# Kernel tuning notes

Measured on AMD Instinct MI355X. Metric: run time of the kernel, lower is better.

## Reference

```python
import jax, jax.numpy as jnp
import numpy as np

K, N = 4096, 4096
GROUP_SIZE = 64
N_GROUPS = N // GROUP_SIZE
B, S = 4, 2048
NBITS = 4


def setup_inputs() -> dict:
    key = jax.random.key(0)
    ks = jax.random.split(key, 7)
    x = jax.random.normal(ks[0], (B, S, N), dtype=jnp.float32)
    # per-group scales/zeros broadcast over the group_size axis
    scales = jax.random.uniform(ks[1], (K, N_GROUPS, 1), dtype=jnp.float32, minval=0.001, maxval=0.05)
    zeros = jax.random.uniform(ks[2], (K, N_GROUPS, 1), dtype=jnp.float32, minval=0.0, maxval=2.0 ** NBITS - 1)
    mu1 = jax.random.uniform(ks[3], (N,), dtype=jnp.float32, minval=0.5, maxval=1.5)
    mu2 = jax.random.uniform(ks[4], (K,), dtype=jnp.float32, minval=0.5, maxval=1.5)
    bias = jax.random.normal(ks[5], (K,), dtype=jnp.float32)
    W_q = jax.random.randint(ks[6], (K, N), 0, 2 ** NBITS, dtype=jnp.int32)
    return {"x": x, "scales": scales, "zeros": zeros, "mu1": mu1, "mu2": mu2, "bias": bias, "W_q": W_q}


def reference(x, scales, zeros, mu1, mu2, bias, W_q):
    # dequantize: per-group (Q - zero) * scale, then Sinkhorn rescale mu2 (rows) * mu1 (cols)
    k, n = W_q.shape
    n_groups = scales.shape[1]
    Qg = W_q.astype(jnp.float32).reshape(k, n_groups, -1)  # [K, G, gs]
    W_deq = ((Qg - zeros) * scales).reshape(k, n) * mu2[:, None] * mu1[None, :]
    W_deq = W_deq.astype(x.dtype)
    # nn.functional.linear: x @ W^T + b
    return jnp.einsum('bsn,kn->bsk', x, W_deq) + bias
```

## Files before the change

kernel.cpp:

```cpp
#include <hip/hip_runtime.h>
#include <hip/hip_bf16.h>
#include <stdint.h>
#include <type_traits>

typedef unsigned short u16;
typedef __bf16 bf16x8 __attribute__((ext_vector_type(8)));
typedef float f32x4 __attribute__((ext_vector_type(4)));

#define M_TOT 8192
#define N_TOT 4096
#define K_TOT 4096
#define BM 256
#define BN 256
#define BK 64
#define NT 64

#define HALF_EL 8192
#define B_OFF   16384
#define SLOT_EL 32768

template <int V> using ic = std::integral_constant<int, V>;
template <bool V> using bc = std::integral_constant<bool, V>;

__device__ __forceinline__ u16 f2bf(float f) {
    union { float f; uint32_t u; } v; v.f = f;
    uint32_t u = v.u;
    return (u16)((u + 0x7fffu + ((u >> 16) & 1u)) >> 16);
}

__global__ __launch_bounds__(256) void cvt_x_kernel(const float* __restrict__ x,
                                                    u16* __restrict__ xb) {
    const int i = blockIdx.x * blockDim.x + threadIdx.x;
    const float4* p = (const float4*)x + (size_t)i * 2;
    float4 v0 = p[0], v1 = p[1];
    uint4 o;
    o.x = (uint32_t)f2bf(v0.x) | ((uint32_t)f2bf(v0.y) << 16);
    o.y = (uint32_t)f2bf(v0.z) | ((uint32_t)f2bf(v0.w) << 16);
    o.z = (uint32_t)f2bf(v1.x) | ((uint32_t)f2bf(v1.y) << 16);
    o.w = (uint32_t)f2bf(v1.z) | ((uint32_t)f2bf(v1.w) << 16);
    *((uint4*)(xb + (size_t)i * 8)) = o;
}

__global__ __launch_bounds__(256) void deq_w_kernel(const int* __restrict__ wq,
                                                    const float* __restrict__ scales,
                                                    const float* __restrict__ zeros,
                                                    const float* __restrict__ mu1,
                                                    const float* __restrict__ mu2,
                                                    u16* __restrict__ wb) {
    const int i = blockIdx.x * blockDim.x + threadIdx.x;
    const int k  = i >> 9;
    const int n0 = (i & 511) << 3;
    const int g  = n0 >> 6;
    const float z  = zeros[k * 64 + g];
    const float sm = scales[k * 64 + g] * mu2[k];
    const int4* qp = (const int4*)(wq + (size_t)k * N_TOT + n0);
    int4 q0 = qp[0], q1 = qp[1];
    const float4* mp = (const float4*)(mu1 + n0);
    float4 u0 = mp[0], u1 = mp[1];
    uint4 o;
    o.x = (uint32_t)f2bf(((float)q0.x - z) * sm * u0.x) |
          ((uint32_t)f2bf(((float)q0.y - z) * sm * u0.y) << 16);
    o.y = (uint32_t)f2bf(((float)q0.z - z) * sm * u0.z) |
          ((uint32_t)f2bf(((float)q0.w - z) * sm * u0.w) << 16);
    o.z = (uint32_t)f2bf(((float)q1.x - z) * sm * u1.x) |
          ((uint32_t)f2bf(((float)q1.y - z) * sm * u1.y) << 16);
    o.w = (uint32_t)f2bf(((float)q1.z - z) * sm * u1.z) |
          ((uint32_t)f2bf(((float)q1.w - z) * sm * u1.w) << 16);
    *((uint4*)(wb + (size_t)k * N_TOT + n0)) = o;
}

__global__ __launch_bounds__(512, 2) void gemm_kernel(const u16* __restrict__ Xb,
                                                      const u16* __restrict__ Wb,
                                                      const float* __restrict__ bias,
                                                      float* __restrict__ out) {
    __shared__ __align__(16) u16 lds[2 * SLOT_EL];

    const int bid = blockIdx.x;
    const int cpx = gridDim.x >> 3;
    const int swz = (bid & 7) * cpx + (bid >> 3);
    const int bm = swz >> 4;
    const int bn = swz & 15;

    const int tid  = threadIdx.x;
    const int w    = tid >> 6;
    const int lane = tid & 63;
    const int wm = w >> 2, wn = w & 3;

    const int scol = (((lane & 7) ^ (lane >> 3)) << 3);
    const u16* aS = Xb + (size_t)(bm * BM + w * 16 + (lane >> 3)) * N_TOT + scol;
    const u16* bS = Wb + (size_t)(bn * BN + w * 16 + (lane >> 3)) * N_TOT + scol;

    auto stageA = [&](int slot, int h, int u) {
        const u16* s = aS + (size_t)(h * 128) * N_TOT + u * BK;
        u16* d = &lds[slot * SLOT_EL + h * HALF_EL + w * 1024];
        __builtin_amdgcn_global_load_lds(
            (const __attribute__((address_space(1))) uint32_t*)s,
            (__attribute__((address_space(3))) uint32_t*)d, 16, 0, 0);
        __builtin_amdgcn_global_load_lds(
            (const __attribute__((address_space(1))) uint32_t*)(s + (size_t)8 * N_TOT),
            (__attribute__((address_space(3))) uint32_t*)(d + 512), 16, 0, 0);
    };
    auto stageB = [&](int slot, int h, int u) {
        const u16* s = bS + (size_t)(h * 128) * N_TOT + u * BK;
        u16* d = &lds[slot * SLOT_EL + B_OFF + h * HALF_EL + w * 1024];
        __builtin_amdgcn_global_load_lds(
            (const __attribute__((address_space(1))) uint32_t*)s,
            (__attribute__((address_space(3))) uint32_t*)d, 16, 0, 0);
        __builtin_amdgcn_global_load_lds(
            (const __attribute__((address_space(1))) uint32_t*)(s + (size_t)8 * N_TOT),
            (__attribute__((address_space(3))) uint32_t*)(d + 512), 16, 0, 0);
    };

    const int cc0 = (((lane >> 4) << 3)) ^ ((lane & 7) << 3);
    const int rA  = ((wm << 4) + (lane & 15)) << 6;
    const int rB  = ((wn << 4) + (lane & 15)) << 6;

    f32x4 acc[2][2][4][2] = {};
    bf16x8 af[2][4][2];
    bf16x8 bf[2][2][2];

    auto phase = [&](auto Pc, auto Sc, auto Wc, int t) {
        constexpr int P = Pc.value;
        constexpr bool S = Sc.value;
        constexpr int W = Wc.value;
        constexpr int mh = P >> 1, nh = P & 1;
        const int slot = (t & 1) * SLOT_EL;
        if constexpr (P == 0 || P == 1) {
            #pragma unroll
            for (int j = 0; j < 4; ++j) {
                af[P][j][0] = *(const bf16x8*)&lds[slot + P * HALF_EL + rA + j * 2048 + cc0];
                af[P][j][1] = *(const bf16x8*)&lds[slot + P * HALF_EL + rA + j * 2048 + (cc0 ^ 32)];
            }
            #pragma unroll
            for (int j2 = 0; j2 < 2; ++j2) {
                bf[P][j2][0] = *(const bf16x8*)&lds[slot + B_OFF + P * HALF_EL + rB + j2 * 4096 + cc0];
                bf[P][j2][1] = *(const bf16x8*)&lds[slot + B_OFF + P * HALF_EL + rB + j2 * 4096 + (cc0 ^ 32)];
            }
        }
        if constexpr (S) {
            if constexpr (P == 0) stageA((t + 1) & 1, 0, t + 1);
            if constexpr (P == 1) stageB((t + 1) & 1, 0, t + 1);
            if constexpr (P == 2) stageA((t + 1) & 1, 1, t + 1);
            if constexpr (P == 3) stageB((t + 1) & 1, 1, t + 1);
        }
        __builtin_amdgcn_s_barrier();
        asm volatile("s_waitcnt lgkmcnt(0)" ::: "memory");
        __builtin_amdgcn_sched_barrier(0);
        __builtin_amdgcn_s_setprio(1);
        #pragma unroll
        for (int j = 0; j < 4; ++j)
            #pragma unroll
            for (int j2 = 0; j2 < 2; ++j2)
                #pragma unroll
                for (int ks = 0; ks < 2; ++ks)
                    acc[mh][nh][j][j2] = __builtin_amdgcn_mfma_f32_16x16x32_bf16(
                        af[mh][j][ks], bf[nh][j2][ks], acc[mh][nh][j][j2], 0, 0, 0);
        __builtin_amdgcn_s_setprio(0);
        if constexpr (W == 0)      asm volatile("s_waitcnt vmcnt(0)" ::: "memory");
        else if constexpr (W == 2) asm volatile("s_waitcnt vmcnt(2)" ::: "memory");
        else if constexpr (W == 4) asm volatile("s_waitcnt vmcnt(4)" ::: "memory");
        __builtin_amdgcn_s_barrier();
    };

    stageA(0, 0, 0); stageB(0, 0, 0); stageA(0, 1, 0); stageB(0, 1, 0);
    asm volatile("s_waitcnt vmcnt(4)" ::: "memory");
    __builtin_amdgcn_s_barrier();

    for (int t = 0; t < NT - 1; ++t) {
        phase(ic<0>{}, bc<true>{}, ic<2>{}, t);
        phase(ic<1>{}, bc<true>{}, ic<-1>{}, t);
        phase(ic<2>{}, bc<true>{}, ic<-1>{}, t);
        phase(ic<3>{}, bc<true>{}, ic<4>{}, t);
    }
    phase(ic<0>{}, bc<false>{}, ic<0>{}, NT - 1);
    phase(ic<1>{}, bc<false>{}, ic<-1>{}, NT - 1);
    phase(ic<2>{}, bc<false>{}, ic<-1>{}, NT - 1);
    phase(ic<3>{}, bc<false>{}, ic<-1>{}, NT - 1);

    #pragma unroll
    for (int mh_ = 0; mh_ < 2; ++mh_)
        #pragma unroll
        for (int j = 0; j < 4; ++j)
            #pragma unroll
            for (int rr = 0; rr < 4; ++rr) {
                const int row = bm * BM + mh_ * 128 + j * 32 + wm * 16 + ((lane >> 4) << 2) + rr;
                float* orow = out + (size_t)row * K_TOT;
                #pragma unroll
                for (int nh_ = 0; nh_ < 2; ++nh_)
                    #pragma unroll
                    for (int j2 = 0; j2 < 2; ++j2) {
                        const int col = bn * BN + nh_ * 128 + j2 * 64 + wn * 16 + (lane & 15);
                        orow[col] = acc[mh_][nh_][j][j2][rr] + bias[col];
                    }
            }
}

extern "C" void kernel_launch(void* const* d_in, const int* in_sizes, int n_in,
                              void* d_out, int out_size, void* d_ws, size_t ws_size,
                              hipStream_t stream) {
    const float* x      = (const float*)d_in[0];
    const float* scales = (const float*)d_in[1];
    const float* zeros  = (const float*)d_in[2];
    const float* mu1    = (const float*)d_in[3];
    const float* mu2    = (const float*)d_in[4];
    const float* bias   = (const float*)d_in[5];
    const int*   wq     = (const int*)d_in[6];
    float* out = (float*)d_out;

    u16* xb = (u16*)d_ws;
    u16* wb = (u16*)d_ws + (size_t)M_TOT * N_TOT;

    cvt_x_kernel<<<(M_TOT * N_TOT / 8) / 256, 256, 0, stream>>>(x, xb);
    deq_w_kernel<<<(K_TOT * N_TOT / 8) / 256, 256, 0, stream>>>(wq, scales, zeros, mu1, mu2, wb);
    gemm_kernel<<<(M_TOT / BM) * (K_TOT / BN), 512, 0, stream>>>(xb, wb, bias, out);
}
```

Baseline: 280.4 us.

## Replace four-phase interleaved GEMM pipeline with a single-barrier double-buffered loop

Drops the templated four-phase schedule, which split each K-step into quarter-tile MFMA groups with staggered A/B prefetches and explicit vmcnt and lgkmcnt waits. In its place is one loop per K tile: a __syncthreads, all LDS fragment reads, a single prefetch of the next tile, then all 64 MFMAs. This cuts the number of barriers per tile and frees the compiler to schedule freely. The cost is the fine-grained overlap between global loads, LDS reads and MFMA issue, and the barrier now relies on __syncthreads draining every outstanding load.

After: 270.8 us. -3.4%, faster.

```diff
diff --git a/kernel.cpp b/kernel.cpp
--- a/kernel.cpp
+++ b/kernel.cpp
@@ -1,7 +1,6 @@
 #include <hip/hip_runtime.h>
 #include <hip/hip_bf16.h>
 #include <stdint.h>
-#include <type_traits>
 
 typedef unsigned short u16;
 typedef __bf16 bf16x8 __attribute__((ext_vector_type(8)));
@@ -18,9 +17,6 @@
 #define HALF_EL 8192
 #define B_OFF   16384
 #define SLOT_EL 32768
-
-template <int V> using ic = std::integral_constant<int, V>;
-template <bool V> using bc = std::integral_constant<bool, V>;
 
 __device__ __forceinline__ u16 f2bf(float f) {
     union { float f; uint32_t u; } v; v.f = f;
@@ -90,25 +86,27 @@
     const u16* aS = Xb + (size_t)(bm * BM + w * 16 + (lane >> 3)) * N_TOT + scol;
     const u16* bS = Wb + (size_t)(bn * BN + w * 16 + (lane >> 3)) * N_TOT + scol;
 
-    auto stageA = [&](int slot, int h, int u) {
-        const u16* s = aS + (size_t)(h * 128) * N_TOT + u * BK;
-        u16* d = &lds[slot * SLOT_EL + h * HALF_EL + w * 1024];
-        __builtin_amdgcn_global_load_lds(
-            (const __attribute__((address_space(1))) uint32_t*)s,
-            (__attribute__((address_space(3))) uint32_t*)d, 16, 0, 0);
-        __builtin_amdgcn_global_load_lds(
-            (const __attribute__((address_space(1))) uint32_t*)(s + (size_t)8 * N_TOT),
-            (__attribute__((address_space(3))) uint32_t*)(d + 512), 16, 0, 0);
-    };
-    auto stageB = [&](int slot, int h, int u) {
-        const u16* s = bS + (size_t)(h * 128) * N_TOT + u * BK;
-        u16* d = &lds[slot * SLOT_EL + B_OFF + h * HALF_EL + w * 1024];
-        __builtin_amdgcn_global_load_lds(
-            (const __attribute__((address_space(1))) uint32_t*)s,
-            (__attribute__((address_space(3))) uint32_t*)d, 16, 0, 0);
-        __builtin_amdgcn_global_load_lds(
-            (const __attribute__((address_space(1))) uint32_t*)(s + (size_t)8 * N_TOT),
-            (__attribute__((address_space(3))) uint32_t*)(d + 512), 16, 0, 0);
+    auto stage_tile = [&](int slot, int u) {
+        u16* base = &lds[slot * SLOT_EL + w * 1024];
+        #pragma unroll
+        for (int h = 0; h < 2; ++h) {
+            const u16* sa = aS + (size_t)(h * 128) * N_TOT + u * BK;
+            const u16* sb = bS + (size_t)(h * 128) * N_TOT + u * BK;
+            u16* da = base + h * HALF_EL;
+            u16* db = base + B_OFF + h * HALF_EL;
+            __builtin_amdgcn_global_load_lds(
+                (const __attribute__((address_space(1))) uint32_t*)sa,
+                (__attribute__((address_space(3))) uint32_t*)da, 16, 0, 0);
+            __builtin_amdgcn_global_load_lds(
+                (const __attribute__((address_space(1))) uint32_t*)(sa + (size_t)8 * N_TOT),
+                (__attribute__((address_space(3))) uint32_t*)(da + 512), 16, 0, 0);
+            __builtin_amdgcn_global_load_lds(
+                (const __attribute__((address_space(1))) uint32_t*)sb,
+                (__attribute__((address_space(3))) uint32_t*)db, 16, 0, 0);
+            __builtin_amdgcn_global_load_lds(
+                (const __attribute__((address_space(1))) uint32_t*)(sb + (size_t)8 * N_TOT),
+                (__attribute__((address_space(3))) uint32_t*)(db + 512), 16, 0, 0);
+        }
     };
 
     const int cc0 = (((lane >> 4) << 3)) ^ ((lane & 7) << 3);
@@ -119,63 +117,70 @@
     bf16x8 af[2][4][2];
     bf16x8 bf[2][2][2];
 
-    auto phase = [&](auto Pc, auto Sc, auto Wc, int t) {
-        constexpr int P = Pc.value;
-        constexpr bool S = Sc.value;
-        constexpr int W = Wc.value;
-        constexpr int mh = P >> 1, nh = P & 1;
+    stage_tile(0, 0);
+
+    for (int t = 0; t < NT; ++t) {
+        __syncthreads();
         const int slot = (t & 1) * SLOT_EL;
-        if constexpr (P == 0 || P == 1) {
-            #pragma unroll
-            for (int j = 0; j < 4; ++j) {
-                af[P][j][0] = *(const bf16x8*)&lds[slot + P * HALF_EL + rA + j * 2048 + cc0];
-                af[P][j][1] = *(const bf16x8*)&lds[slot + P * HALF_EL + rA + j * 2048 + (cc0 ^ 32)];
-            }
-            #pragma unroll
-            for (int j2 = 0; j2 < 2; ++j2) {
-                bf[P][j2][0] = *(const bf16x8*)&lds[slot + B_OFF + P * HALF_EL + rB + j2 * 4096 + cc0];
-                bf[P][j2][1] = *(const bf16x8*)&lds[slot + B_OFF + P * HALF_EL + rB + j2 * 4096 + (cc0 ^ 32)];
-            }
-        }
-        if constexpr (S) {
-            if constexpr (P == 0) stageA((t + 1) & 1, 0, t + 1);
-            if constexpr (P == 1) stageB((t + 1) & 1, 0, t + 1);
-            if constexpr (P == 2) stageA((t + 1) & 1, 1, t + 1);
-            if constexpr (P == 3) stageB((t + 1) & 1, 1, t + 1);
-        }
-        __builtin_amdgcn_s_barrier();
-        asm volatile("s_waitcnt lgkmcnt(0)" ::: "memory");
-        __builtin_amdgcn_sched_barrier(0);
+
+        #pragma unroll
+        for (int j = 0; j < 4; ++j) {
+            af[0][j][0] = *(const bf16x8*)&lds[slot + rA + j * 2048 + cc0];
+            af[0][j][1] = *(const bf16x8*)&lds[slot + rA + j * 2048 + (cc0 ^ 32)];
+        }
+        #pragma unroll
+        for (int j2 = 0; j2 < 2; ++j2) {
+            bf[0][j2][0] = *(const bf16x8*)&lds[slot + B_OFF + rB + j2 * 4096 + cc0];
+            bf[0][j2][1] = *(const bf16x8*)&lds[slot + B_OFF + rB + j2 * 4096 + (cc0 ^ 32)];
+        }
+        #pragma unroll
+        for (int j = 0; j < 4; ++j) {
+            af[1][j][0] = *(const bf16x8*)&lds[slot + HALF_EL + rA + j * 2048 + cc0];
+            af[1][j][1] = *(const bf16x8*)&lds[slot + HALF_EL + rA + j * 2048 + (cc0 ^ 32)];
+        }
+        #pragma unroll
+        for (int j2 = 0; j2 < 2; ++j2) {
+            bf[1][j2][0] = *(const bf16x8*)&lds[slot + B_OFF + HALF_EL + rB + j2 * 4096 + cc0];
+            bf[1][j2][1] = *(const bf16x8*)&lds[slot + B_OFF + HALF_EL + rB + j2 * 4096 + (cc0 ^ 32)];
+        }
+
+        if (t < NT - 1) stage_tile((t + 1) & 1, t + 1);
+
         __builtin_amdgcn_s_setprio(1);
         #pragma unroll
-        for (int j = 0; j < 4; ++j)
-            #pragma unroll
-            for (int j2 = 0; j2 < 2; ++j2)
-                #pragma unroll
-                for (int ks = 0; ks < 2; ++ks)
-                    acc[mh][nh][j][j2] = __builtin_amdgcn_mfma_f32_16x16x32_bf16(
-                        af[mh][j][ks], bf[nh][j2][ks], acc[mh][nh][j][j2], 0, 0, 0);
+        for (int ks = 0; ks < 2; ++ks)
+            #pragma unroll
+            for (int j = 0; j < 4; ++j)
+                #pragma unroll
+                for (int j2 = 0; j2 < 2; ++j2)
+                    acc[0][0][j][j2] = __builtin_amdgcn_mfma_f32_16x16x32_bf16(
+                        af[0][j][ks], bf[0][j2][ks], acc[0][0][j][j2], 0, 0, 0);
+        #pragma unroll
+        for (int ks = 0; ks < 2; ++ks)
+            #pragma unroll
+            for (int j = 0; j < 4; ++j)
+                #pragma unroll
+                for (int j2 = 0; j2 < 2; ++j2)
+                    acc[1][0][j][j2] = __builtin_amdgcn_mfma_f32_16x16x32_bf16(
+                        af[1][j][ks], bf[0][j2][ks], acc[1][0][j][j2], 0, 0, 0);
+        #pragma unroll
+        for (int ks = 0; ks < 2; ++ks)
+            #pragma unroll
+            for (int j = 0; j < 4; ++j)
+                #pragma unroll
+                for (int j2 = 0; j2 < 2; ++j2)
+                    acc[0][1][j][j2] = __builtin_amdgcn_mfma_f32_16x16x32_bf16(
+                        af[0][j][ks], bf[1][j2][ks], acc[0][1][j][j2], 0, 0, 0);
+        #pragma unroll
+        for (int ks = 0; ks < 2; ++ks)
+            #pragma unroll
+            for (int j = 0; j < 4; ++j)
+                #pragma unroll
+                for (int j2 = 0; j2 < 2; ++j2)
+                    acc[1][1][j][j2] = __builtin_amdgcn_mfma_f32_16x16x32_bf16(
+                        af[1][j][ks], bf[1][j2][ks], acc[1][1][j][j2], 0, 0, 0);
         __builtin_amdgcn_s_setprio(0);
-        if constexpr (W == 0)      asm volatile("s_waitcnt vmcnt(0)" ::: "memory");
-        else if constexpr (W == 2) asm volatile("s_waitcnt vmcnt(2)" ::: "memory");
-        else if constexpr (W == 4) asm volatile("s_waitcnt vmcnt(4)" ::: "memory");
-        __builtin_amdgcn_s_barrier();
-    };
-
-    stageA(0, 0, 0); stageB(0, 0, 0); stageA(0, 1, 0); stageB(0, 1, 0);
-    asm volatile("s_waitcnt vmcnt(4)" ::: "memory");
-    __builtin_amdgcn_s_barrier();
-
-    for (int t = 0; t < NT - 1; ++t) {
-        phase(ic<0>{}, bc<true>{}, ic<2>{}, t);
-        phase(ic<1>{}, bc<true>{}, ic<-1>{}, t);
-        phase(ic<2>{}, bc<true>{}, ic<-1>{}, t);
-        phase(ic<3>{}, bc<true>{}, ic<4>{}, t);
     }
-    phase(ic<0>{}, bc<false>{}, ic<0>{}, NT - 1);
-    phase(ic<1>{}, bc<false>{}, ic<-1>{}, NT - 1);
-    phase(ic<2>{}, bc<false>{}, ic<-1>{}, NT - 1);
-    phase(ic<3>{}, bc<false>{}, ic<-1>{}, NT - 1);
 
     #pragma unroll
     for (int mh_ = 0; mh_ < 2; ++mh_)
```

## Reorder GEMM phases into serpentine order with deeper cross-tile prefetch

Applied to the files above, without the earlier changes.

Changes the four-phase quadrant order to a serpentine (0,0),(0,1),(1,1),(1,0) so each phase loads only one new fragment set (A or B half) from LDS instead of both. Reschedules the global-to-LDS staging so halves for tile t+2 are issued into the slot freed within tile t, with a prologue that preloads most of tile 1, and relaxes vmcnt waits to keep more loads in flight. MFMA loop order is changed to iterate ks outermost. This adds runtime branches on t in the loop and relies on subtle slot-reuse timing, so a misplaced wait could race.

Result: no change. 278.2 us (-0.8%).

```diff
diff --git a/kernel.cpp b/kernel.cpp
--- a/kernel.cpp
+++ b/kernel.cpp
@@ -20,7 +20,6 @@
 #define SLOT_EL 32768
 
 template <int V> using ic = std::integral_constant<int, V>;
-template <bool V> using bc = std::integral_constant<bool, V>;
 
 __device__ __forceinline__ u16 f2bf(float f) {
     union { float f; uint32_t u; } v; v.f = f;
@@ -117,65 +116,78 @@
 
     f32x4 acc[2][2][4][2] = {};
     bf16x8 af[2][4][2];
-    bf16x8 bf[2][2][2];
-
-    auto phase = [&](auto Pc, auto Sc, auto Wc, int t) {
+    bf16x8 bfr[2][2][2];
+
+    auto phase = [&](auto Pc, int t) {
         constexpr int P = Pc.value;
-        constexpr bool S = Sc.value;
-        constexpr int W = Wc.value;
-        constexpr int mh = P >> 1, nh = P & 1;
+        constexpr int mh = (P >= 2) ? 1 : 0;
+        constexpr int nh = (P == 1 || P == 2) ? 1 : 0;
         const int slot = (t & 1) * SLOT_EL;
-        if constexpr (P == 0 || P == 1) {
+
+        if constexpr (P == 0) {
             #pragma unroll
             for (int j = 0; j < 4; ++j) {
-                af[P][j][0] = *(const bf16x8*)&lds[slot + P * HALF_EL + rA + j * 2048 + cc0];
-                af[P][j][1] = *(const bf16x8*)&lds[slot + P * HALF_EL + rA + j * 2048 + (cc0 ^ 32)];
+                af[0][j][0] = *(const bf16x8*)&lds[slot + rA + j * 2048 + cc0];
+                af[0][j][1] = *(const bf16x8*)&lds[slot + rA + j * 2048 + (cc0 ^ 32)];
             }
             #pragma unroll
             for (int j2 = 0; j2 < 2; ++j2) {
-                bf[P][j2][0] = *(const bf16x8*)&lds[slot + B_OFF + P * HALF_EL + rB + j2 * 4096 + cc0];
-                bf[P][j2][1] = *(const bf16x8*)&lds[slot + B_OFF + P * HALF_EL + rB + j2 * 4096 + (cc0 ^ 32)];
+                bfr[0][j2][0] = *(const bf16x8*)&lds[slot + B_OFF + rB + j2 * 4096 + cc0];
+                bfr[0][j2][1] = *(const bf16x8*)&lds[slot + B_OFF + rB + j2 * 4096 + (cc0 ^ 32)];
+            }
+        } else if constexpr (P == 1) {
+            #pragma unroll
+            for (int j2 = 0; j2 < 2; ++j2) {
+                bfr[1][j2][0] = *(const bf16x8*)&lds[slot + B_OFF + HALF_EL + rB + j2 * 4096 + cc0];
+                bfr[1][j2][1] = *(const bf16x8*)&lds[slot + B_OFF + HALF_EL + rB + j2 * 4096 + (cc0 ^ 32)];
+            }
+        } else if constexpr (P == 2) {
+            #pragma unroll
+            for (int j = 0; j < 4; ++j) {
+                af[1][j][0] = *(const bf16x8*)&lds[slot + HALF_EL + rA + j * 2048 + cc0];
+                af[1][j][1] = *(const bf16x8*)&lds[slot + HALF_EL + rA + j * 2048 + (cc0 ^ 32)];
             }
         }
-        if constexpr (S) {
-            if constexpr (P == 0) stageA((t + 1) & 1, 0, t + 1);
-            if constexpr (P == 1) stageB((t + 1) & 1, 0, t + 1);
-            if constexpr (P == 2) stageA((t + 1) & 1, 1, t + 1);
-            if constexpr (P == 3) stageB((t + 1) & 1, 1, t + 1);
-        }
+
+        if constexpr (P == 0) { if (t + 1 < NT) stageA((t + 1) & 1, 1, t + 1); }
+        if constexpr (P == 1) { if (t + 2 < NT) stageA(t & 1, 0, t + 2); }
+        if constexpr (P == 2) { if (t + 2 < NT) stageB(t & 1, 0, t + 2); }
+        if constexpr (P == 3) { if (t + 2 < NT) stageB(t & 1, 1, t + 2); }
+
+        if constexpr (P == 0)
+            asm volatile("s_waitcnt lgkmcnt(8)" ::: "memory");
+
         __builtin_amdgcn_s_barrier();
         asm volatile("s_waitcnt lgkmcnt(0)" ::: "memory");
         __builtin_amdgcn_sched_barrier(0);
         __builtin_amdgcn_s_setprio(1);
         #pragma unroll
-        for (int j = 0; j < 4; ++j)
-            #pragma unroll
-            for (int j2 = 0; j2 < 2; ++j2)
+        for (int ks = 0; ks < 2; ++ks)
+            #pragma unroll
+            for (int j = 0; j < 4; ++j)
                 #pragma unroll
-                for (int ks = 0; ks < 2; ++ks)
+                for (int j2 = 0; j2 < 2; ++j2)
                     acc[mh][nh][j][j2] = __builtin_amdgcn_mfma_f32_16x16x32_bf16(
-                        af[mh][j][ks], bf[nh][j2][ks], acc[mh][nh][j][j2], 0, 0, 0);
+                        af[mh][j][ks], bfr[nh][j2][ks], acc[mh][nh][j][j2], 0, 0, 0);
         __builtin_amdgcn_s_setprio(0);
-        if constexpr (W == 0)      asm volatile("s_waitcnt vmcnt(0)" ::: "memory");
-        else if constexpr (W == 2) asm volatile("s_waitcnt vmcnt(2)" ::: "memory");
-        else if constexpr (W == 4) asm volatile("s_waitcnt vmcnt(4)" ::: "memory");
+        if constexpr (P == 3) {
+            if (t < NT - 2) asm volatile("s_waitcnt vmcnt(6)" ::: "memory");
+            else            asm volatile("s_waitcnt vmcnt(0)" ::: "memory");
+        }
         __builtin_amdgcn_s_barrier();
     };
 
-    stageA(0, 0, 0); stageB(0, 0, 0); stageA(0, 1, 0); stageB(0, 1, 0);
-    asm volatile("s_waitcnt vmcnt(4)" ::: "memory");
+    stageA(0, 0, 0); stageB(0, 0, 0); stageB(0, 1, 0); stageA(0, 1, 0);
+    stageA(1, 0, 1); stageB(1, 0, 1); stageB(1, 1, 1);
+    asm volatile("s_waitcnt vmcnt(6)" ::: "memory");
     __builtin_amdgcn_s_barrier();
 
-    for (int t = 0; t < NT - 1; ++t) {
-        phase(ic<0>{}, bc<true>{}, ic<2>{}, t);
-        phase(ic<1>{}, bc<true>{}, ic<-1>{}, t);
-        phase(ic<2>{}, bc<true>{}, ic<-1>{}, t);
-        phase(ic<3>{}, bc<true>{}, ic<4>{}, t);
+    for (int t = 0; t < NT; ++t) {
+        phase(ic<0>{}, t);
+        phase(ic<1>{}, t);
+        phase(ic<2>{}, t);
+        phase(ic<3>{}, t);
     }
-    phase(ic<0>{}, bc<false>{}, ic<0>{}, NT - 1);
-    phase(ic<1>{}, bc<false>{}, ic<-1>{}, NT - 1);
-    phase(ic<2>{}, bc<false>{}, ic<-1>{}, NT - 1);
-    phase(ic<3>{}, bc<false>{}, ic<-1>{}, NT - 1);
 
     #pragma unroll
     for (int mh_ = 0; mh_ < 2; ++mh_)
```
